# Kernel tuning notes

Hardware: AMD Instinct MI355X
Metric: run time of the kernel (lower is better)

The kernel has to match this reference:

```python
import jax, jax.numpy as jnp
import numpy as np

HID = 256
IN_DIM = 64
OUT_DIM = 4
B = 2048
T = 128


def setup_inputs() -> dict:
    key = jax.random.key(0)
    ks = jax.random.split(key, 12)
    s = lambda k, shp, fan: jax.random.normal(k, shp, jnp.float32) / np.sqrt(fan)
    return {
        "static_input": jax.random.normal(ks[0], (B, IN_DIM), jnp.float32),
        "times": jnp.arange(T, dtype=jnp.float32) * 0.05,  # increasing grid
        "W_in": s(ks[1], (IN_DIM, HID), IN_DIM), "b_in": jnp.zeros((HID,), jnp.float32),
        "W1": s(ks[2], (HID, HID), HID), "b1": jnp.zeros((HID,), jnp.float32),
        "W2": s(ks[3], (HID, HID), HID), "b2": jnp.zeros((HID,), jnp.float32),
        "W_pk": s(ks[4], (HID, OUT_DIM), HID), "b_pk": jnp.zeros((OUT_DIM,), jnp.float32),
        "W_pd": s(ks[5], (HID, 1), HID), "b_pd": jnp.zeros((1,), jnp.float32),
    }


def _odefunc(h, W1, b1, W2, b2):
    # Linear -> Tanh -> Linear (autonomous: ignores t, as in the torch ODEFunc)
    return jnp.tanh(h @ W1 + b1) @ W2 + b2


def reference(static_input, times, W_in, b_in, W1, b1, W2, b2, W_pk, b_pk, W_pd, b_pd):
    h0 = static_input @ W_in + b_in  # [B, H]
    f = lambda h: _odefunc(h, W1, b1, W2, b2)
    dts = times[1:] - times[:-1]  # [T-1]

    def rk4_step(h, dt):
        k1 = f(h)
        k2 = f(h + 0.5 * dt * k1)
        k3 = f(h + 0.5 * dt * k2)
        k4 = f(h + dt * k3)
        h_next = h + (dt / 6.0) * (k1 + 2.0 * k2 + 2.0 * k3 + k4)
        return h_next, h_next

    _, h_rest = jax.lax.scan(rk4_step, h0, dts)  # [T-1, B, H]
    h_ts = jnp.concatenate([h0[None], h_rest], axis=0)  # [T, B, H]
    h_ts = jnp.transpose(h_ts, (1, 0, 2))  # [B, T, H]
    pk_pred = h_ts @ W_pk + b_pk          # [B, T, OUT_DIM]
    pd_pred = h_ts[:, -1, :] @ W_pd + b_pd  # [B, 1]
    return (pk_pred, pd_pred)
```

## Files before the change

### kernel.cpp

```cpp
#include <hip/hip_runtime.h>
#include <hip/hip_bf16.h>
#include <stdint.h>

#define H       256
#define INDIM   64
#define TSTEPS  128
#define BATCH   2048
#define MROWS   8
#define OUTD    4

typedef __attribute__((ext_vector_type(8))) short bf16x8;
typedef __attribute__((ext_vector_type(4))) float f32x4;

__device__ __forceinline__ short b2s(float x) {
  __hip_bfloat16 h = __float2bfloat16(x);
  return __builtin_bit_cast(short, h);
}

__device__ __forceinline__ int swz(int m, int n) {
  return (m * H + n) ^ ((m & 7) << 3);
}

__device__ __forceinline__ float swap_hilo(float a, float b) {
#if __has_builtin(__builtin_amdgcn_permlane32_swap)
  typedef unsigned int u32x2 __attribute__((ext_vector_type(2)));
  u32x2 r = __builtin_amdgcn_permlane32_swap(
      __builtin_bit_cast(unsigned int, a),
      __builtin_bit_cast(unsigned int, b), false, false);
  return __builtin_bit_cast(float, r[0]);
#else
  float t = __shfl_xor(b, 32);
  return (threadIdx.x & 32) ? t : a;
#endif
}

__global__ __launch_bounds__(512, 1) void node_kernel(
    const float* __restrict__ g_static, const float* __restrict__ g_times,
    const float* __restrict__ g_Win, const float* __restrict__ g_bin,
    const float* __restrict__ g_W1, const float* __restrict__ g_b1,
    const float* __restrict__ g_W2, const float* __restrict__ g_b2,
    const float* __restrict__ g_Wpk, const float* __restrict__ g_bpk,
    const float* __restrict__ g_Wpd, const float* __restrict__ g_bpd,
    float* __restrict__ g_out)
{
  __shared__ __align__(16) short arg_lds[MROWS * H];
  __shared__ __align__(16) short h1_lds[MROWS * H];
  __shared__ __align__(16) short wpk_lds[8 * 64 * 8];
  __shared__ float h_lds[MROWS * H];
  __shared__ float s_lds[MROWS * INDIM];
  __shared__ float t_lds[TSTEPS];

  const int tid   = threadIdx.x;
  const int lane  = tid & 63;
  const int wid   = tid >> 6;
  const int g     = lane >> 4;
  const int c     = lane & 15;
  const int b0    = blockIdx.x * MROWS;
  const int ncol0 = wid * 32;
  const int am    = lane & 7;
  const int gg    = (lane >> 4) & 1;
  const int hh    = lane >> 5;
  const int colu  = ncol0 + 16 * hh + c;
  const int dm    = 4 * g;

  if (tid < TSTEPS) t_lds[tid] = g_times[tid];

  const float b1u2 = 2.0f * g_b1[colu];
  const float b2u  = g_b2[colu];
  const float bpkc = g_bpk[c & 3];
  const float bpdv = g_bpd[0];
  float wpd[4];
#pragma unroll
  for (int j = 0; j < 4; ++j) wpd[j] = g_Wpd[lane + 64 * j];

  int ra[8], wa[4], ha[4];
#pragma unroll
  for (int kt = 0; kt < 8; ++kt) ra[kt] = swz(am, kt * 32 + g * 8);
#pragma unroll
  for (int r = 0; r < 4; ++r) {
    wa[r] = swz(4 * gg + r, colu);
    ha[r] = (4 * gg + r) * H + colu;
  }

  bf16x8 w1f[8][2], w2f[8][2];
#pragma unroll
  for (int kt = 0; kt < 8; ++kt) {
#pragma unroll
    for (int nt = 0; nt < 2; ++nt) {
      const int n  = ncol0 + nt * 16 + c;
      const int kb = kt * 32 + g * 8;
      bf16x8 f1, f2;
#pragma unroll
      for (int u = 0; u < 8; ++u) {
        f1[u] = b2s(g_W1[(kb + u) * H + n]);
        f2[u] = b2s(g_W2[(kb + u) * H + n]);
      }
      w1f[kt][nt] = f1;
      w2f[kt][nt] = f2;
    }
  }

  if (wid == 0) {
#pragma unroll
    for (int kt = 0; kt < 8; ++kt) {
      bf16x8 f;
#pragma unroll
      for (int u = 0; u < 8; ++u) {
        const int k = kt * 32 + g * 8 + u;
        f[u] = (c < OUTD) ? b2s(g_Wpk[k * OUTD + c]) : (short)0;
      }
      *(bf16x8*)(wpk_lds + kt * 512 + lane * 8) = f;
    }
  }

  s_lds[tid] = g_static[(b0 + (tid >> 6)) * INDIM + (tid & 63)];
  __syncthreads();
  {
    const int m  = tid >> 6;
    const int n0 = (tid & 63) * 4;
    float a0 = g_bin[n0], a1 = g_bin[n0 + 1], a2 = g_bin[n0 + 2], a3 = g_bin[n0 + 3];
#pragma unroll 8
    for (int k = 0; k < INDIM; ++k) {
      const float sv = s_lds[m * INDIM + k];
      const f32x4 w = *(const f32x4*)(g_Win + k * H + n0);
      a0 += sv * w[0]; a1 += sv * w[1]; a2 += sv * w[2]; a3 += sv * w[3];
    }
    h_lds[m * H + n0] = a0;     h_lds[m * H + n0 + 1] = a1;
    h_lds[m * H + n0 + 2] = a2; h_lds[m * H + n0 + 3] = a3;
    arg_lds[swz(m, n0)]     = b2s(a0);
    arg_lds[swz(m, n0 + 1)] = b2s(a1);
    arg_lds[swz(m, n0 + 2)] = b2s(a2);
    arg_lds[swz(m, n0 + 3)] = b2s(a3);
  }
  __syncthreads();

  float hb[4];
#pragma unroll
  for (int r = 0; r < 4; ++r) hb[r] = h_lds[ha[r]];

  auto emit_pk = [&](int t) {
    if (wid == 0) {
      f32x4 acc = {0.f, 0.f, 0.f, 0.f};
#pragma unroll
      for (int kt = 0; kt < 8; ++kt) {
        const bf16x8 aA = *(const bf16x8*)(arg_lds + ra[kt]);
        const bf16x8 bW = *(const bf16x8*)(wpk_lds + kt * 512 + lane * 8);
        acc = __builtin_amdgcn_mfma_f32_16x16x32_bf16(aA, bW, acc, 0, 0, 0);
      }
      if (g < 2 && c < OUTD) {
#pragma unroll
        for (int r = 0; r < 4; ++r)
          g_out[((size_t)(b0 + dm + r) * TSTEPS + t) * OUTD + c] = acc[r] + bpkc;
      }
    }
  };

  emit_pk(0);

  for (int t = 1; t < TSTEPS; ++t) {
    const float dt = t_lds[t] - t_lds[t - 1];
    const float s6 = dt * (1.0f / 6.0f);
    float ks[4];

#pragma unroll
    for (int ev = 0; ev < 4; ++ev) {
      f32x4 A0 = {0.f,0.f,0.f,0.f}, A1 = {0.f,0.f,0.f,0.f};
      f32x4 B0 = {0.f,0.f,0.f,0.f}, B1 = {0.f,0.f,0.f,0.f};
#pragma unroll
      for (int kt = 0; kt < 4; ++kt) {
        const bf16x8 aA = *(const bf16x8*)(arg_lds + ra[kt]);
        const bf16x8 aB = *(const bf16x8*)(arg_lds + ra[kt + 4]);
        A0 = __builtin_amdgcn_mfma_f32_16x16x32_bf16(aA, w1f[kt][0], A0, 0, 0, 0);
        A1 = __builtin_amdgcn_mfma_f32_16x16x32_bf16(aA, w1f[kt][1], A1, 0, 0, 0);
        B0 = __builtin_amdgcn_mfma_f32_16x16x32_bf16(aB, w1f[kt + 4][0], B0, 0, 0, 0);
        B1 = __builtin_amdgcn_mfma_f32_16x16x32_bf16(aB, w1f[kt + 4][1], B1, 0, 0, 0);
      }
#pragma unroll
      for (int r = 0; r < 4; ++r) {
        const float v = swap_hilo(A0[r] + B0[r], A1[r] + B1[r]);
        const float e = __expf(__builtin_fmaf(2.0f, v, b1u2));
        const float th = 1.0f - __fdividef(2.0f, e + 1.0f);
        h1_lds[wa[r]] = b2s(th);
      }
      __syncthreads();

      A0 = f32x4{0.f,0.f,0.f,0.f}; A1 = f32x4{0.f,0.f,0.f,0.f};
      B0 = f32x4{0.f,0.f,0.f,0.f}; B1 = f32x4{0.f,0.f,0.f,0.f};
#pragma unroll
      for (int kt = 0; kt < 4; ++kt) {
        const bf16x8 aA = *(const bf16x8*)(h1_lds + ra[kt]);
        const bf16x8 aB = *(const bf16x8*)(h1_lds + ra[kt + 4]);
        A0 = __builtin_amdgcn_mfma_f32_16x16x32_bf16(aA, w2f[kt][0], A0, 0, 0, 0);
        A1 = __builtin_amdgcn_mfma_f32_16x16x32_bf16(aA, w2f[kt][1], A1, 0, 0, 0);
        B0 = __builtin_amdgcn_mfma_f32_16x16x32_bf16(aB, w2f[kt + 4][0], B0, 0, 0, 0);
        B1 = __builtin_amdgcn_mfma_f32_16x16x32_bf16(aB, w2f[kt + 4][1], B1, 0, 0, 0);
      }
#pragma unroll
      for (int r = 0; r < 4; ++r) {
        const float kv = swap_hilo(A0[r] + B0[r], A1[r] + B1[r]) + b2u;
        if (ev == 0)      ks[r] = kv;
        else if (ev == 3) ks[r] += kv;
        else              ks[r] += 2.0f * kv;
        if (ev < 3) {
          const float cc = (ev == 2) ? dt : 0.5f * dt;
          arg_lds[wa[r]] = b2s(__builtin_fmaf(cc, kv, hb[r]));
        } else {
          hb[r] = __builtin_fmaf(s6, ks[r], hb[r]);
          arg_lds[wa[r]] = b2s(hb[r]);
        }
      }
      __syncthreads();
    }
    emit_pk(t);
  }

#pragma unroll
  for (int r = 0; r < 4; ++r) h_lds[ha[r]] = hb[r];
  __syncthreads();
  {
    float p = 0.0f;
#pragma unroll
    for (int j = 0; j < 4; ++j) p += h_lds[wid * H + lane + 64 * j] * wpd[j];
#pragma unroll
    for (int m = 1; m < 64; m <<= 1) p += __shfl_xor(p, m);
    if (lane == 0) g_out[(size_t)BATCH * TSTEPS * OUTD + b0 + wid] = p + bpdv;
  }
}

extern "C" void kernel_launch(void* const* d_in, const int* in_sizes, int n_in,
                              void* d_out, int out_size, void* d_ws, size_t ws_size,
                              hipStream_t stream) {
  const float* g_static = (const float*)d_in[0];
  const float* g_times  = (const float*)d_in[1];
  const float* g_Win    = (const float*)d_in[2];
  const float* g_bin    = (const float*)d_in[3];
  const float* g_W1     = (const float*)d_in[4];
  const float* g_b1     = (const float*)d_in[5];
  const float* g_W2     = (const float*)d_in[6];
  const float* g_b2     = (const float*)d_in[7];
  const float* g_Wpk    = (const float*)d_in[8];
  const float* g_bpk    = (const float*)d_in[9];
  const float* g_Wpd    = (const float*)d_in[10];
  const float* g_bpd    = (const float*)d_in[11];

  node_kernel<<<dim3(BATCH / MROWS), dim3(512), 0, stream>>>(
      g_static, g_times, g_Win, g_bin, g_W1, g_b1, g_W2, g_b2,
      g_Wpk, g_bpk, g_Wpd, g_bpd, (float*)d_out);
}
```

Measured before the change: 660.7 us.

## Re-swizzle LDS layout for conflict-free loads and split MFMA accumulators into four chains

Replaces the XOR swizzle of the bf16 activation buffers with a new grouped index mapping, and permutes the Wpk LDS slots to match, aiming to remove LDS bank conflicts on the 16-byte fragment loads. The MFMA reduction now hoists all eight A-fragment loads up front and spreads the K dimension over four independent accumulator chains per output tile instead of two, to shorten dependent MFMA latency within each RK4 stage. This costs extra accumulator registers and a final vector add tree, and the new swizzle must stay consistent across all readers and writers.

```diff
diff --git a/kernel.cpp b/kernel.cpp
--- a/kernel.cpp
+++ b/kernel.cpp
@@ -17,8 +17,16 @@
   return __builtin_bit_cast(short, h);
 }
 
-__device__ __forceinline__ int swz(int m, int n) {
-  return (m * H + n) ^ ((m & 7) << 3);
+__device__ __forceinline__ int grp(int row, int kt, int g) {
+  return (((row ^ g) & 3) << 1) | (((g >> 1) ^ kt ^ (row >> 2)) & 1);
+}
+__device__ __forceinline__ int sidx(int row, int col) {
+  const int kt = col >> 5, g = (col >> 3) & 3, u = col & 7;
+  return row * 256 + ((kt >> 1) << 6) + grp(row, kt, g) * 8 + u;
+}
+__device__ __forceinline__ int wpk_slot(int lane) {
+  return (((lane & 3) << 1) | ((lane >> 4) & 1)) |
+         (((lane >> 2) & 3) << 3) | (((lane >> 5) & 1) << 5);
 }
 
 __device__ __forceinline__ float swap_hilo(float a, float b) {
@@ -33,6 +41,8 @@
   return (threadIdx.x & 32) ? t : a;
 #endif
 }
+
+#define MFMA(a, b, c) __builtin_amdgcn_mfma_f32_16x16x32_bf16((a), (b), (c), 0, 0, 0)
 
 __global__ __launch_bounds__(512, 1) void node_kernel(
     const float* __restrict__ g_static, const float* __restrict__ g_times,
@@ -75,10 +85,10 @@
 
   int ra[8], wa[4], ha[4];
 #pragma unroll
-  for (int kt = 0; kt < 8; ++kt) ra[kt] = swz(am, kt * 32 + g * 8);
+  for (int kt = 0; kt < 8; ++kt) ra[kt] = sidx(am, kt * 32 + g * 8);
 #pragma unroll
   for (int r = 0; r < 4; ++r) {
-    wa[r] = swz(4 * gg + r, colu);
+    wa[r] = sidx(4 * gg + r, colu);
     ha[r] = (4 * gg + r) * H + colu;
   }
 
@@ -101,6 +111,7 @@
   }
 
   if (wid == 0) {
+    const int slot = wpk_slot(lane);
 #pragma unroll
     for (int kt = 0; kt < 8; ++kt) {
       bf16x8 f;
@@ -109,7 +120,7 @@
         const int k = kt * 32 + g * 8 + u;
         f[u] = (c < OUTD) ? b2s(g_Wpk[k * OUTD + c]) : (short)0;
       }
-      *(bf16x8*)(wpk_lds + kt * 512 + lane * 8) = f;
+      *(bf16x8*)(wpk_lds + kt * 512 + slot * 8) = f;
     }
   }
 
@@ -127,10 +138,10 @@
     }
     h_lds[m * H + n0] = a0;     h_lds[m * H + n0 + 1] = a1;
     h_lds[m * H + n0 + 2] = a2; h_lds[m * H + n0 + 3] = a3;
-    arg_lds[swz(m, n0)]     = b2s(a0);
-    arg_lds[swz(m, n0 + 1)] = b2s(a1);
-    arg_lds[swz(m, n0 + 2)] = b2s(a2);
-    arg_lds[swz(m, n0 + 3)] = b2s(a3);
+    arg_lds[sidx(m, n0)]     = b2s(a0);
+    arg_lds[sidx(m, n0 + 1)] = b2s(a1);
+    arg_lds[sidx(m, n0 + 2)] = b2s(a2);
+    arg_lds[sidx(m, n0 + 3)] = b2s(a3);
   }
   __syncthreads();
 
@@ -138,14 +149,15 @@
 #pragma unroll
   for (int r = 0; r < 4; ++r) hb[r] = h_lds[ha[r]];
 
+  const int wslot = wpk_slot(lane);
   auto emit_pk = [&](int t) {
     if (wid == 0) {
       f32x4 acc = {0.f, 0.f, 0.f, 0.f};
 #pragma unroll
       for (int kt = 0; kt < 8; ++kt) {
         const bf16x8 aA = *(const bf16x8*)(arg_lds + ra[kt]);
-        const bf16x8 bW = *(const bf16x8*)(wpk_lds + kt * 512 + lane * 8);
-        acc = __builtin_amdgcn_mfma_f32_16x16x32_bf16(aA, bW, acc, 0, 0, 0);
+        const bf16x8 bW = *(const bf16x8*)(wpk_lds + kt * 512 + wslot * 8);
+        acc = MFMA(aA, bW, acc);
       }
       if (g < 2 && c < OUTD) {
 #pragma unroll
@@ -157,6 +169,7 @@
 
   emit_pk(0);
 
+  const f32x4 vz = {0.f, 0.f, 0.f, 0.f};
   for (int t = 1; t < TSTEPS; ++t) {
     const float dt = t_lds[t] - t_lds[t - 1];
     const float s6 = dt * (1.0f / 6.0f);
@@ -164,49 +177,71 @@
 
 #pragma unroll
     for (int ev = 0; ev < 4; ++ev) {
-      f32x4 A0 = {0.f,0.f,0.f,0.f}, A1 = {0.f,0.f,0.f,0.f};
-      f32x4 B0 = {0.f,0.f,0.f,0.f}, B1 = {0.f,0.f,0.f,0.f};
-#pragma unroll
-      for (int kt = 0; kt < 4; ++kt) {
-        const bf16x8 aA = *(const bf16x8*)(arg_lds + ra[kt]);
-        const bf16x8 aB = *(const bf16x8*)(arg_lds + ra[kt + 4]);
-        A0 = __builtin_amdgcn_mfma_f32_16x16x32_bf16(aA, w1f[kt][0], A0, 0, 0, 0);
-        A1 = __builtin_amdgcn_mfma_f32_16x16x32_bf16(aA, w1f[kt][1], A1, 0, 0, 0);
-        B0 = __builtin_amdgcn_mfma_f32_16x16x32_bf16(aB, w1f[kt + 4][0], B0, 0, 0, 0);
-        B1 = __builtin_amdgcn_mfma_f32_16x16x32_bf16(aB, w1f[kt + 4][1], B1, 0, 0, 0);
-      }
-#pragma unroll
-      for (int r = 0; r < 4; ++r) {
-        const float v = swap_hilo(A0[r] + B0[r], A1[r] + B1[r]);
-        const float e = __expf(__builtin_fmaf(2.0f, v, b1u2));
-        const float th = 1.0f - __fdividef(2.0f, e + 1.0f);
-        h1_lds[wa[r]] = b2s(th);
+      {
+        const bf16x8 f0 = *(const bf16x8*)(arg_lds + ra[0]);
+        const bf16x8 f1 = *(const bf16x8*)(arg_lds + ra[1]);
+        const bf16x8 f2 = *(const bf16x8*)(arg_lds + ra[2]);
+        const bf16x8 f3 = *(const bf16x8*)(arg_lds + ra[3]);
+        const bf16x8 f4 = *(const bf16x8*)(arg_lds + ra[4]);
+        const bf16x8 f5 = *(const bf16x8*)(arg_lds + ra[5]);
+        const bf16x8 f6 = *(const bf16x8*)(arg_lds + ra[6]);
+        const bf16x8 f7 = *(const bf16x8*)(arg_lds + ra[7]);
+        f32x4 c00 = vz, c01 = vz, c02 = vz, c03 = vz;
+        f32x4 c10 = vz, c11 = vz, c12 = vz, c13 = vz;
+        c00 = MFMA(f0, w1f[0][0], c00); c10 = MFMA(f0, w1f[0][1], c10);
+        c01 = MFMA(f2, w1f[2][0], c01); c11 = MFMA(f2, w1f[2][1], c11);
+        c02 = MFMA(f4, w1f[4][0], c02); c12 = MFMA(f4, w1f[4][1], c12);
+        c03 = MFMA(f6, w1f[6][0], c03); c13 = MFMA(f6, w1f[6][1], c13);
+        c00 = MFMA(f1, w1f[1][0], c00); c10 = MFMA(f1, w1f[1][1], c10);
+        c01 = MFMA(f3, w1f[3][0], c01); c11 = MFMA(f3, w1f[3][1], c11);
+        c02 = MFMA(f5, w1f[5][0], c02); c12 = MFMA(f5, w1f[5][1], c12);
+        c03 = MFMA(f7, w1f[7][0], c03); c13 = MFMA(f7, w1f[7][1], c13);
+        const f32x4 S0 = (c00 + c01) + (c02 + c03);
+        const f32x4 S1 = (c10 + c11) + (c12 + c13);
+#pragma unroll
+        for (int r = 0; r < 4; ++r) {
+          const float v = swap_hilo(S0[r], S1[r]);
+          const float e = __expf(__builtin_fmaf(2.0f, v, b1u2));
+          const float th = 1.0f - __fdividef(2.0f, e + 1.0f);
+          h1_lds[wa[r]] = b2s(th);
+        }
       }
       __syncthreads();
 
-      A0 = f32x4{0.f,0.f,0.f,0.f}; A1 = f32x4{0.f,0.f,0.f,0.f};
-      B0 = f32x4{0.f,0.f,0.f,0.f}; B1 = f32x4{0.f,0.f,0.f,0.f};
-#pragma unroll
-      for (int kt = 0; kt < 4; ++kt) {
-        const bf16x8 aA = *(const bf16x8*)(h1_lds + ra[kt]);
-        const bf16x8 aB = *(const bf16x8*)(h1_lds + ra[kt + 4]);
-        A0 = __builtin_amdgcn_mfma_f32_16x16x32_bf16(aA, w2f[kt][0], A0, 0, 0, 0);
-        A1 = __builtin_amdgcn_mfma_f32_16x16x32_bf16(aA, w2f[kt][1], A1, 0, 0, 0);
-        B0 = __builtin_amdgcn_mfma_f32_16x16x32_bf16(aB, w2f[kt + 4][0], B0, 0, 0, 0);
-        B1 = __builtin_amdgcn_mfma_f32_16x16x32_bf16(aB, w2f[kt + 4][1], B1, 0, 0, 0);
-      }
-#pragma unroll
-      for (int r = 0; r < 4; ++r) {
-        const float kv = swap_hilo(A0[r] + B0[r], A1[r] + B1[r]) + b2u;
-        if (ev == 0)      ks[r] = kv;
-        else if (ev == 3) ks[r] += kv;
-        else              ks[r] += 2.0f * kv;
-        if (ev < 3) {
-          const float cc = (ev == 2) ? dt : 0.5f * dt;
-          arg_lds[wa[r]] = b2s(__builtin_fmaf(cc, kv, hb[r]));
-        } else {
-          hb[r] = __builtin_fmaf(s6, ks[r], hb[r]);
-          arg_lds[wa[r]] = b2s(hb[r]);
+      {
+        const bf16x8 f0 = *(const bf16x8*)(h1_lds + ra[0]);
+        const bf16x8 f1 = *(const bf16x8*)(h1_lds + ra[1]);
+        const bf16x8 f2 = *(const bf16x8*)(h1_lds + ra[2]);
+        const bf16x8 f3 = *(const bf16x8*)(h1_lds + ra[3]);
+        const bf16x8 f4 = *(const bf16x8*)(h1_lds + ra[4]);
+        const bf16x8 f5 = *(const bf16x8*)(h1_lds + ra[5]);
+        const bf16x8 f6 = *(const bf16x8*)(h1_lds + ra[6]);
+        const bf16x8 f7 = *(const bf16x8*)(h1_lds + ra[7]);
+        f32x4 c00 = vz, c01 = vz, c02 = vz, c03 = vz;
+        f32x4 c10 = vz, c11 = vz, c12 = vz, c13 = vz;
+        c00 = MFMA(f0, w2f[0][0], c00); c10 = MFMA(f0, w2f[0][1], c10);
+        c01 = MFMA(f2, w2f[2][0], c01); c11 = MFMA(f2, w2f[2][1], c11);
+        c02 = MFMA(f4, w2f[4][0], c02); c12 = MFMA(f4, w2f[4][1], c12);
+        c03 = MFMA(f6, w2f[6][0], c03); c13 = MFMA(f6, w2f[6][1], c13);
+        c00 = MFMA(f1, w2f[1][0], c00); c10 = MFMA(f1, w2f[1][1], c10);
+        c01 = MFMA(f3, w2f[3][0], c01); c11 = MFMA(f3, w2f[3][1], c11);
+        c02 = MFMA(f5, w2f[5][0], c02); c12 = MFMA(f5, w2f[5][1], c12);
+        c03 = MFMA(f7, w2f[7][0], c03); c13 = MFMA(f7, w2f[7][1], c13);
+        const f32x4 S0 = (c00 + c01) + (c02 + c03);
+        const f32x4 S1 = (c10 + c11) + (c12 + c13);
+#pragma unroll
+        for (int r = 0; r < 4; ++r) {
+          const float kv = swap_hilo(S0[r], S1[r]) + b2u;
+          if (ev == 0)      ks[r] = kv;
+          else if (ev == 3) ks[r] += kv;
+          else              ks[r] += 2.0f * kv;
+          if (ev < 3) {
+            const float cc = (ev == 2) ? dt : 0.5f * dt;
+            arg_lds[wa[r]] = b2s(__builtin_fmaf(cc, kv, hb[r]));
+          } else {
+            hb[r] = __builtin_fmaf(s6, ks[r], hb[r]);
+            arg_lds[wa[r]] = b2s(hb[r]);
+          }
         }
       }
       __syncthreads();
```

Result: slower. 724.1 us (+9.6%).

## Halve block to 4 waves, each computing 64 columns with doubled register weights

Applied to the files above, without the earlier changes.

The block shrinks from 8 to 4 waves. Each wave now owns 64 output columns and holds 8x4 bf16 fragments of W1 and W2 in registers, with several pieces of state (hb, ks, write addresses) doubled to match. Biases are folded into the MFMA accumulator init instead of being added afterwards. The W_pk LDS slot mapping is permuted, and the input projection and final pd reduction are adjusted for 256 threads. The aim is to cut barrier and LDS-fragment-reload overhead per RK4 stage by giving each wave more MFMAs per A-fragment load. The cost is much higher VGPR pressure (256 weight vector registers) and less parallelism per block, which risks spills.

```diff
diff --git a/kernel.cpp b/kernel.cpp
--- a/kernel.cpp
+++ b/kernel.cpp
@@ -19,6 +19,10 @@
 
 __device__ __forceinline__ int swz(int m, int n) {
   return (m * H + n) ^ ((m & 7) << 3);
+}
+__device__ __forceinline__ int wpk_slot(int lane) {
+  return (((lane & 3) << 1) | ((lane >> 4) & 1)) |
+         (((lane >> 2) & 3) << 3) | (((lane >> 5) & 1) << 5);
 }
 
 __device__ __forceinline__ float swap_hilo(float a, float b) {
@@ -34,7 +38,9 @@
 #endif
 }
 
-__global__ __launch_bounds__(512, 1) void node_kernel(
+#define MFMA(a, b, c) __builtin_amdgcn_mfma_f32_16x16x32_bf16((a), (b), (c), 0, 0, 0)
+
+__global__ __launch_bounds__(256, 1) void node_kernel(
     const float* __restrict__ g_static, const float* __restrict__ g_times,
     const float* __restrict__ g_Win, const float* __restrict__ g_bin,
     const float* __restrict__ g_W1, const float* __restrict__ g_b1,
@@ -56,37 +62,43 @@
   const int g     = lane >> 4;
   const int c     = lane & 15;
   const int b0    = blockIdx.x * MROWS;
-  const int ncol0 = wid * 32;
+  const int ncol0 = wid * 64;
   const int am    = lane & 7;
   const int gg    = (lane >> 4) & 1;
   const int hh    = lane >> 5;
-  const int colu  = ncol0 + 16 * hh + c;
+  const int cu    = ncol0 + 16 * hh + c;
   const int dm    = 4 * g;
 
   if (tid < TSTEPS) t_lds[tid] = g_times[tid];
 
-  const float b1u2 = 2.0f * g_b1[colu];
-  const float b2u  = g_b2[colu];
+  float b1v[4], b2v[4];
+#pragma unroll
+  for (int nt = 0; nt < 4; ++nt) {
+    b1v[nt] = g_b1[ncol0 + nt * 16 + c];
+    b2v[nt] = g_b2[ncol0 + nt * 16 + c];
+  }
   const float bpkc = g_bpk[c & 3];
   const float bpdv = g_bpd[0];
   float wpd[4];
 #pragma unroll
   for (int j = 0; j < 4; ++j) wpd[j] = g_Wpd[lane + 64 * j];
 
-  int ra[8], wa[4], ha[4];
+  int ra[8], wa[2][4], ha[2][4];
 #pragma unroll
   for (int kt = 0; kt < 8; ++kt) ra[kt] = swz(am, kt * 32 + g * 8);
 #pragma unroll
-  for (int r = 0; r < 4; ++r) {
-    wa[r] = swz(4 * gg + r, colu);
-    ha[r] = (4 * gg + r) * H + colu;
-  }
-
-  bf16x8 w1f[8][2], w2f[8][2];
+  for (int p = 0; p < 2; ++p)
+#pragma unroll
+    for (int r = 0; r < 4; ++r) {
+      wa[p][r] = swz(4 * gg + r, cu + 32 * p);
+      ha[p][r] = (4 * gg + r) * H + cu + 32 * p;
+    }
+
+  bf16x8 w1f[8][4], w2f[8][4];
 #pragma unroll
   for (int kt = 0; kt < 8; ++kt) {
 #pragma unroll
-    for (int nt = 0; nt < 2; ++nt) {
+    for (int nt = 0; nt < 4; ++nt) {
       const int n  = ncol0 + nt * 16 + c;
       const int kb = kt * 32 + g * 8;
       bf16x8 f1, f2;
@@ -101,6 +113,7 @@
   }
 
   if (wid == 0) {
+    const int slot = wpk_slot(lane);
 #pragma unroll
     for (int kt = 0; kt < 8; ++kt) {
       bf16x8 f;
@@ -109,43 +122,53 @@
         const int k = kt * 32 + g * 8 + u;
         f[u] = (c < OUTD) ? b2s(g_Wpk[k * OUTD + c]) : (short)0;
       }
-      *(bf16x8*)(wpk_lds + kt * 512 + lane * 8) = f;
-    }
-  }
-
-  s_lds[tid] = g_static[(b0 + (tid >> 6)) * INDIM + (tid & 63)];
+      *(bf16x8*)(wpk_lds + kt * 512 + slot * 8) = f;
+    }
+  }
+
+  s_lds[tid]       = g_static[(b0 + (tid >> 6)) * INDIM + (tid & 63)];
+  s_lds[tid + 256] = g_static[(b0 + ((tid + 256) >> 6)) * INDIM + (tid & 63)];
   __syncthreads();
   {
-    const int m  = tid >> 6;
-    const int n0 = (tid & 63) * 4;
-    float a0 = g_bin[n0], a1 = g_bin[n0 + 1], a2 = g_bin[n0 + 2], a3 = g_bin[n0 + 3];
-#pragma unroll 8
+    const int m  = tid >> 5;
+    const int n0 = (tid & 31) * 8;
+    float a[8];
+#pragma unroll
+    for (int j = 0; j < 8; ++j) a[j] = g_bin[n0 + j];
+#pragma unroll 4
     for (int k = 0; k < INDIM; ++k) {
       const float sv = s_lds[m * INDIM + k];
-      const f32x4 w = *(const f32x4*)(g_Win + k * H + n0);
-      a0 += sv * w[0]; a1 += sv * w[1]; a2 += sv * w[2]; a3 += sv * w[3];
-    }
-    h_lds[m * H + n0] = a0;     h_lds[m * H + n0 + 1] = a1;
-    h_lds[m * H + n0 + 2] = a2; h_lds[m * H + n0 + 3] = a3;
-    arg_lds[swz(m, n0)]     = b2s(a0);
-    arg_lds[swz(m, n0 + 1)] = b2s(a1);
-    arg_lds[swz(m, n0 + 2)] = b2s(a2);
-    arg_lds[swz(m, n0 + 3)] = b2s(a3);
+      const f32x4 w0 = *(const f32x4*)(g_Win + k * H + n0);
+      const f32x4 w1 = *(const f32x4*)(g_Win + k * H + n0 + 4);
+#pragma unroll
+      for (int j = 0; j < 4; ++j) {
+        a[j]     += sv * w0[j];
+        a[j + 4] += sv * w1[j];
+      }
+    }
+#pragma unroll
+    for (int j = 0; j < 8; ++j) {
+      h_lds[m * H + n0 + j]     = a[j];
+      arg_lds[swz(m, n0 + j)]   = b2s(a[j]);
+    }
   }
   __syncthreads();
 
-  float hb[4];
-#pragma unroll
-  for (int r = 0; r < 4; ++r) hb[r] = h_lds[ha[r]];
-
+  float hb[2][4];
+#pragma unroll
+  for (int p = 0; p < 2; ++p)
+#pragma unroll
+    for (int r = 0; r < 4; ++r) hb[p][r] = h_lds[ha[p][r]];
+
+  const int wslot = wpk_slot(lane);
   auto emit_pk = [&](int t) {
     if (wid == 0) {
       f32x4 acc = {0.f, 0.f, 0.f, 0.f};
 #pragma unroll
       for (int kt = 0; kt < 8; ++kt) {
         const bf16x8 aA = *(const bf16x8*)(arg_lds + ra[kt]);
-        const bf16x8 bW = *(const bf16x8*)(wpk_lds + kt * 512 + lane * 8);
-        acc = __builtin_amdgcn_mfma_f32_16x16x32_bf16(aA, bW, acc, 0, 0, 0);
+        const bf16x8 bW = *(const bf16x8*)(wpk_lds + kt * 512 + wslot * 8);
+        acc = MFMA(aA, bW, acc);
       }
       if (g < 2 && c < OUTD) {
 #pragma unroll
@@ -157,57 +180,82 @@
 
   emit_pk(0);
 
+  const f32x4 vz = {0.f, 0.f, 0.f, 0.f};
   for (int t = 1; t < TSTEPS; ++t) {
     const float dt = t_lds[t] - t_lds[t - 1];
     const float s6 = dt * (1.0f / 6.0f);
-    float ks[4];
+    float ks[2][4];
 
 #pragma unroll
     for (int ev = 0; ev < 4; ++ev) {
-      f32x4 A0 = {0.f,0.f,0.f,0.f}, A1 = {0.f,0.f,0.f,0.f};
-      f32x4 B0 = {0.f,0.f,0.f,0.f}, B1 = {0.f,0.f,0.f,0.f};
-#pragma unroll
-      for (int kt = 0; kt < 4; ++kt) {
-        const bf16x8 aA = *(const bf16x8*)(arg_lds + ra[kt]);
-        const bf16x8 aB = *(const bf16x8*)(arg_lds + ra[kt + 4]);
-        A0 = __builtin_amdgcn_mfma_f32_16x16x32_bf16(aA, w1f[kt][0], A0, 0, 0, 0);
-        A1 = __builtin_amdgcn_mfma_f32_16x16x32_bf16(aA, w1f[kt][1], A1, 0, 0, 0);
-        B0 = __builtin_amdgcn_mfma_f32_16x16x32_bf16(aB, w1f[kt + 4][0], B0, 0, 0, 0);
-        B1 = __builtin_amdgcn_mfma_f32_16x16x32_bf16(aB, w1f[kt + 4][1], B1, 0, 0, 0);
-      }
-#pragma unroll
-      for (int r = 0; r < 4; ++r) {
-        const float v = swap_hilo(A0[r] + B0[r], A1[r] + B1[r]);
-        const float e = __expf(__builtin_fmaf(2.0f, v, b1u2));
-        const float th = 1.0f - __fdividef(2.0f, e + 1.0f);
-        h1_lds[wa[r]] = b2s(th);
+      {
+        f32x4 cA[4], cB[4];
+#pragma unroll
+        for (int nt = 0; nt < 4; ++nt) {
+          cA[nt] = f32x4{b1v[nt], b1v[nt], b1v[nt], b1v[nt]};
+          cB[nt] = vz;
+        }
+#pragma unroll
+        for (int kt = 0; kt < 4; ++kt) {
+          const bf16x8 fA = *(const bf16x8*)(arg_lds + ra[kt]);
+          const bf16x8 fB = *(const bf16x8*)(arg_lds + ra[kt + 4]);
+#pragma unroll
+          for (int nt = 0; nt < 4; ++nt) {
+            cA[nt] = MFMA(fA, w1f[kt][nt], cA[nt]);
+            cB[nt] = MFMA(fB, w1f[kt + 4][nt], cB[nt]);
+          }
+        }
+        f32x4 S[4];
+#pragma unroll
+        for (int nt = 0; nt < 4; ++nt) S[nt] = cA[nt] + cB[nt];
+#pragma unroll
+        for (int p = 0; p < 2; ++p)
+#pragma unroll
+          for (int r = 0; r < 4; ++r) {
+            const float v = swap_hilo(S[2 * p][r], S[2 * p + 1][r]);
+            const float e = __expf(2.0f * v);
+            const float th = 1.0f - __fdividef(2.0f, e + 1.0f);
+            h1_lds[wa[p][r]] = b2s(th);
+          }
       }
       __syncthreads();
 
-      A0 = f32x4{0.f,0.f,0.f,0.f}; A1 = f32x4{0.f,0.f,0.f,0.f};
-      B0 = f32x4{0.f,0.f,0.f,0.f}; B1 = f32x4{0.f,0.f,0.f,0.f};
-#pragma unroll
-      for (int kt = 0; kt < 4; ++kt) {
-        const bf16x8 aA = *(const bf16x8*)(h1_lds + ra[kt]);
-        const bf16x8 aB = *(const bf16x8*)(h1_lds + ra[kt + 4]);
-        A0 = __builtin_amdgcn_mfma_f32_16x16x32_bf16(aA, w2f[kt][0], A0, 0, 0, 0);
-        A1 = __builtin_amdgcn_mfma_f32_16x16x32_bf16(aA, w2f[kt][1], A1, 0, 0, 0);
-        B0 = __builtin_amdgcn_mfma_f32_16x16x32_bf16(aB, w2f[kt + 4][0], B0, 0, 0, 0);
-        B1 = __builtin_amdgcn_mfma_f32_16x16x32_bf16(aB, w2f[kt + 4][1], B1, 0, 0, 0);
-      }
-#pragma unroll
-      for (int r = 0; r < 4; ++r) {
-        const float kv = swap_hilo(A0[r] + B0[r], A1[r] + B1[r]) + b2u;
-        if (ev == 0)      ks[r] = kv;
-        else if (ev == 3) ks[r] += kv;
-        else              ks[r] += 2.0f * kv;
-        if (ev < 3) {
-          const float cc = (ev == 2) ? dt : 0.5f * dt;
-          arg_lds[wa[r]] = b2s(__builtin_fmaf(cc, kv, hb[r]));
-        } else {
-          hb[r] = __builtin_fmaf(s6, ks[r], hb[r]);
-          arg_lds[wa[r]] = b2s(hb[r]);
+      {
+        f32x4 cA[4], cB[4];
+#pragma unroll
+        for (int nt = 0; nt < 4; ++nt) {
+          cA[nt] = f32x4{b2v[nt], b2v[nt], b2v[nt], b2v[nt]};
+          cB[nt] = vz;
         }
+#pragma unroll
+        for (int kt = 0; kt < 4; ++kt) {
+          const bf16x8 fA = *(const bf16x8*)(h1_lds + ra[kt]);
+          const bf16x8 fB = *(const bf16x8*)(h1_lds + ra[kt + 4]);
+#pragma unroll
+          for (int nt = 0; nt < 4; ++nt) {
+            cA[nt] = MFMA(fA, w2f[kt][nt], cA[nt]);
+            cB[nt] = MFMA(fB, w2f[kt + 4][nt], cB[nt]);
+          }
+        }
+        f32x4 S[4];
+#pragma unroll
+        for (int nt = 0; nt < 4; ++nt) S[nt] = cA[nt] + cB[nt];
+#pragma unroll
+        for (int p = 0; p < 2; ++p)
+#pragma unroll
+          for (int r = 0; r < 4; ++r) {
+            const float kv = swap_hilo(S[2 * p][r], S[2 * p + 1][r]);
+            if (ev == 0)      ks[p][r] = kv;
+            else if (ev == 3) ks[p][r] += kv;
+            else              ks[p][r] += 2.0f * kv;
+            if (ev < 3) {
+              const float cc = (ev == 2) ? dt : 0.5f * dt;
+              arg_lds[wa[p][r]] = b2s(__builtin_fmaf(cc, kv, hb[p][r]));
+            } else {
+              hb[p][r] = __builtin_fmaf(s6, ks[p][r], hb[p][r]);
+              arg_lds[wa[p][r]] = b2s(hb[p][r]);
+            }
+          }
       }
       __syncthreads();
     }
@@ -215,15 +263,19 @@
   }
 
 #pragma unroll
-  for (int r = 0; r < 4; ++r) h_lds[ha[r]] = hb[r];
+  for (int p = 0; p < 2; ++p)
+#pragma unroll
+    for (int r = 0; r < 4; ++r) h_lds[ha[p][r]] = hb[p][r];
   __syncthreads();
-  {
+#pragma unroll
+  for (int rr = 0; rr < 2; ++rr) {
+    const int row = wid + 4 * rr;
     float p = 0.0f;
 #pragma unroll
-    for (int j = 0; j < 4; ++j) p += h_lds[wid * H + lane + 64 * j] * wpd[j];
+    for (int j = 0; j < 4; ++j) p += h_lds[row * H + lane + 64 * j] * wpd[j];
 #pragma unroll
     for (int m = 1; m < 64; m <<= 1) p += __shfl_xor(p, m);
-    if (lane == 0) g_out[(size_t)BATCH * TSTEPS * OUTD + b0 + wid] = p + bpdv;
+    if (lane == 0) g_out[(size_t)BATCH * TSTEPS * OUTD + b0 + row] = p + bpdv;
   }
 }
 
@@ -243,7 +295,7 @@
   const float* g_Wpd    = (const float*)d_in[10];
   const float* g_bpd    = (const float*)d_in[11];
 
-  node_kernel<<<dim3(BATCH / MROWS), dim3(512), 0, stream>>>(
+  node_kernel<<<dim3(BATCH / MROWS), dim3(256), 0, stream>>>(
       g_static, g_times, g_Win, g_bin, g_W1, g_b1, g_W2, g_b2,
       g_Wpk, g_bpk, g_Wpd, g_bpd, (float*)d_out);
 }
```

Result: slower. 924.1 us (+39.9%).

## Duplicate activation rows in LDS, new swizzle, and stagger K order per wave

Applied to the files above, without the earlier changes.

The bf16 activation buffers grow from 8 to 16 rows, with every row written twice so all 16 MFMA A-operand lanes read distinct addresses, and a new XOR swizzle folds the high row bit in. Odd-numbered waves walk the K tiles in rotated order and the register-resident weight fragments are permuted to match, which spreads LDS reads across banks between waves. The Wpk fragment slots are also permuted. This aims to cut LDS bank conflicts on the serial RK4 critical path, at the cost of doubling every LDS store.

```diff
diff --git a/kernel.cpp b/kernel.cpp
--- a/kernel.cpp
+++ b/kernel.cpp
@@ -17,8 +17,13 @@
   return __builtin_bit_cast(short, h);
 }
 
-__device__ __forceinline__ int swz(int m, int n) {
-  return (m * H + n) ^ ((m & 7) << 3);
+__device__ __forceinline__ int sidx16(int m, int n) {
+  const int smix = ((m & 7) ^ (m >> 3)) & 7;
+  return m * H + (n ^ (smix << 3));
+}
+__device__ __forceinline__ int wpk_slot(int lane) {
+  return (((lane & 3) << 1) | ((lane >> 4) & 1)) |
+         (((lane >> 2) & 3) << 3) | (((lane >> 5) & 1) << 5);
 }
 
 __device__ __forceinline__ float swap_hilo(float a, float b) {
@@ -34,6 +39,8 @@
 #endif
 }
 
+#define MFMA(a, b, c) __builtin_amdgcn_mfma_f32_16x16x32_bf16((a), (b), (c), 0, 0, 0)
+
 __global__ __launch_bounds__(512, 1) void node_kernel(
     const float* __restrict__ g_static, const float* __restrict__ g_times,
     const float* __restrict__ g_Win, const float* __restrict__ g_bin,
@@ -43,8 +50,8 @@
     const float* __restrict__ g_Wpd, const float* __restrict__ g_bpd,
     float* __restrict__ g_out)
 {
-  __shared__ __align__(16) short arg_lds[MROWS * H];
-  __shared__ __align__(16) short h1_lds[MROWS * H];
+  __shared__ __align__(16) short arg_lds[16 * H];
+  __shared__ __align__(16) short h1_lds[16 * H];
   __shared__ __align__(16) short wpk_lds[8 * 64 * 8];
   __shared__ float h_lds[MROWS * H];
   __shared__ float s_lds[MROWS * INDIM];
@@ -57,7 +64,7 @@
   const int c     = lane & 15;
   const int b0    = blockIdx.x * MROWS;
   const int ncol0 = wid * 32;
-  const int am    = lane & 7;
+  const int am    = lane & 15;
   const int gg    = (lane >> 4) & 1;
   const int hh    = lane >> 5;
   const int colu  = ncol0 + 16 * hh + c;
@@ -73,18 +80,25 @@
 #pragma unroll
   for (int j = 0; j < 4; ++j) wpd[j] = g_Wpd[lane + 64 * j];
 
-  int ra[8], wa[4], ha[4];
-#pragma unroll
-  for (int kt = 0; kt < 8; ++kt) ra[kt] = swz(am, kt * 32 + g * 8);
+  const int ko = (wid & 1) ? 4 : 0;
+  int ra[8];
+#pragma unroll
+  for (int i = 0; i < 4; ++i) {
+    ra[i]     = sidx16(am, (ko + i) * 32 + g * 8);
+    ra[i + 4] = sidx16(am, ((ko ^ 4) + i) * 32 + g * 8);
+  }
+  int wlo[4], whi[4], ha[4];
 #pragma unroll
   for (int r = 0; r < 4; ++r) {
-    wa[r] = swz(4 * gg + r, colu);
-    ha[r] = (4 * gg + r) * H + colu;
+    wlo[r] = sidx16(4 * gg + r, colu);
+    whi[r] = sidx16(4 * gg + r + 8, colu);
+    ha[r]  = (4 * gg + r) * H + colu;
   }
 
   bf16x8 w1f[8][2], w2f[8][2];
 #pragma unroll
-  for (int kt = 0; kt < 8; ++kt) {
+  for (int i = 0; i < 8; ++i) {
+    const int kt = (i < 4) ? (ko + i) : ((ko ^ 4) + i - 4);
 #pragma unroll
     for (int nt = 0; nt < 2; ++nt) {
       const int n  = ncol0 + nt * 16 + c;
@@ -95,12 +109,13 @@
         f1[u] = b2s(g_W1[(kb + u) * H + n]);
         f2[u] = b2s(g_W2[(kb + u) * H + n]);
       }
-      w1f[kt][nt] = f1;
-      w2f[kt][nt] = f2;
+      w1f[i][nt] = f1;
+      w2f[i][nt] = f2;
     }
   }
 
   if (wid == 0) {
+    const int slot = wpk_slot(lane);
 #pragma unroll
     for (int kt = 0; kt < 8; ++kt) {
       bf16x8 f;
@@ -109,7 +124,7 @@
         const int k = kt * 32 + g * 8 + u;
         f[u] = (c < OUTD) ? b2s(g_Wpk[k * OUTD + c]) : (short)0;
       }
-      *(bf16x8*)(wpk_lds + kt * 512 + lane * 8) = f;
+      *(bf16x8*)(wpk_lds + kt * 512 + slot * 8) = f;
     }
   }
 
@@ -127,10 +142,12 @@
     }
     h_lds[m * H + n0] = a0;     h_lds[m * H + n0 + 1] = a1;
     h_lds[m * H + n0 + 2] = a2; h_lds[m * H + n0 + 3] = a3;
-    arg_lds[swz(m, n0)]     = b2s(a0);
-    arg_lds[swz(m, n0 + 1)] = b2s(a1);
-    arg_lds[swz(m, n0 + 2)] = b2s(a2);
-    arg_lds[swz(m, n0 + 3)] = b2s(a3);
+    const float av[4] = {a0, a1, a2, a3};
+#pragma unroll
+    for (int j = 0; j < 4; ++j) {
+      arg_lds[sidx16(m, n0 + j)]     = b2s(av[j]);
+      arg_lds[sidx16(m + 8, n0 + j)] = b2s(av[j]);
+    }
   }
   __syncthreads();
 
@@ -138,14 +155,15 @@
 #pragma unroll
   for (int r = 0; r < 4; ++r) hb[r] = h_lds[ha[r]];
 
+  const int wslot = wpk_slot(lane);
   auto emit_pk = [&](int t) {
     if (wid == 0) {
       f32x4 acc = {0.f, 0.f, 0.f, 0.f};
 #pragma unroll
       for (int kt = 0; kt < 8; ++kt) {
         const bf16x8 aA = *(const bf16x8*)(arg_lds + ra[kt]);
-        const bf16x8 bW = *(const bf16x8*)(wpk_lds + kt * 512 + lane * 8);
-        acc = __builtin_amdgcn_mfma_f32_16x16x32_bf16(aA, bW, acc, 0, 0, 0);
+        const bf16x8 bW = *(const bf16x8*)(wpk_lds + kt * 512 + wslot * 8);
+        acc = MFMA(aA, bW, acc);
       }
       if (g < 2 && c < OUTD) {
 #pragma unroll
@@ -157,6 +175,7 @@
 
   emit_pk(0);
 
+  const f32x4 vz = {0.f, 0.f, 0.f, 0.f};
   for (int t = 1; t < TSTEPS; ++t) {
     const float dt = t_lds[t] - t_lds[t - 1];
     const float s6 = dt * (1.0f / 6.0f);
@@ -164,49 +183,60 @@
 
 #pragma unroll
     for (int ev = 0; ev < 4; ++ev) {
-      f32x4 A0 = {0.f,0.f,0.f,0.f}, A1 = {0.f,0.f,0.f,0.f};
-      f32x4 B0 = {0.f,0.f,0.f,0.f}, B1 = {0.f,0.f,0.f,0.f};
-#pragma unroll
-      for (int kt = 0; kt < 4; ++kt) {
-        const bf16x8 aA = *(const bf16x8*)(arg_lds + ra[kt]);
-        const bf16x8 aB = *(const bf16x8*)(arg_lds + ra[kt + 4]);
-        A0 = __builtin_amdgcn_mfma_f32_16x16x32_bf16(aA, w1f[kt][0], A0, 0, 0, 0);
-        A1 = __builtin_amdgcn_mfma_f32_16x16x32_bf16(aA, w1f[kt][1], A1, 0, 0, 0);
-        B0 = __builtin_amdgcn_mfma_f32_16x16x32_bf16(aB, w1f[kt + 4][0], B0, 0, 0, 0);
-        B1 = __builtin_amdgcn_mfma_f32_16x16x32_bf16(aB, w1f[kt + 4][1], B1, 0, 0, 0);
-      }
-#pragma unroll
-      for (int r = 0; r < 4; ++r) {
-        const float v = swap_hilo(A0[r] + B0[r], A1[r] + B1[r]);
-        const float e = __expf(__builtin_fmaf(2.0f, v, b1u2));
-        const float th = 1.0f - __fdividef(2.0f, e + 1.0f);
-        h1_lds[wa[r]] = b2s(th);
+      {
+        f32x4 A0 = vz, A1 = vz, B0 = vz, B1 = vz;
+#pragma unroll
+        for (int i = 0; i < 4; ++i) {
+          const bf16x8 fA = *(const bf16x8*)(arg_lds + ra[i]);
+          const bf16x8 fB = *(const bf16x8*)(arg_lds + ra[i + 4]);
+          A0 = MFMA(fA, w1f[i][0], A0);
+          A1 = MFMA(fA, w1f[i][1], A1);
+          B0 = MFMA(fB, w1f[i + 4][0], B0);
+          B1 = MFMA(fB, w1f[i + 4][1], B1);
+        }
+        const f32x4 S0 = A0 + B0;
+        const f32x4 S1 = A1 + B1;
+#pragma unroll
+        for (int r = 0; r < 4; ++r) {
+          const float v  = swap_hilo(S0[r], S1[r]);
+          const float e  = __expf(__builtin_fmaf(2.0f, v, b1u2));
+          const float th = 1.0f - __fdividef(2.0f, e + 1.0f);
+          const short sv = b2s(th);
+          h1_lds[wlo[r]] = sv;
+          h1_lds[whi[r]] = sv;
+        }
       }
       __syncthreads();
 
-      A0 = f32x4{0.f,0.f,0.f,0.f}; A1 = f32x4{0.f,0.f,0.f,0.f};
-      B0 = f32x4{0.f,0.f,0.f,0.f}; B1 = f32x4{0.f,0.f,0.f,0.f};
-#pragma unroll
-      for (int kt = 0; kt < 4; ++kt) {
-        const bf16x8 aA = *(const bf16x8*)(h1_lds + ra[kt]);
-        const bf16x8 aB = *(const bf16x8*)(h1_lds + ra[kt + 4]);
-        A0 = __builtin_amdgcn_mfma_f32_16x16x32_bf16(aA, w2f[kt][0], A0, 0, 0, 0);
-        A1 = __builtin_amdgcn_mfma_f32_16x16x32_bf16(aA, w2f[kt][1], A1, 0, 0, 0);
-        B0 = __builtin_amdgcn_mfma_f32_16x16x32_bf16(aB, w2f[kt + 4][0], B0, 0, 0, 0);
-        B1 = __builtin_amdgcn_mfma_f32_16x16x32_bf16(aB, w2f[kt + 4][1], B1, 0, 0, 0);
-      }
-#pragma unroll
-      for (int r = 0; r < 4; ++r) {
-        const float kv = swap_hilo(A0[r] + B0[r], A1[r] + B1[r]) + b2u;
-        if (ev == 0)      ks[r] = kv;
-        else if (ev == 3) ks[r] += kv;
-        else              ks[r] += 2.0f * kv;
-        if (ev < 3) {
-          const float cc = (ev == 2) ? dt : 0.5f * dt;
-          arg_lds[wa[r]] = b2s(__builtin_fmaf(cc, kv, hb[r]));
-        } else {
-          hb[r] = __builtin_fmaf(s6, ks[r], hb[r]);
-          arg_lds[wa[r]] = b2s(hb[r]);
+      {
+        f32x4 A0 = vz, A1 = vz, B0 = vz, B1 = vz;
+#pragma unroll
+        for (int i = 0; i < 4; ++i) {
+          const bf16x8 fA = *(const bf16x8*)(h1_lds + ra[i]);
+          const bf16x8 fB = *(const bf16x8*)(h1_lds + ra[i + 4]);
+          A0 = MFMA(fA, w2f[i][0], A0);
+          A1 = MFMA(fA, w2f[i][1], A1);
+          B0 = MFMA(fB, w2f[i + 4][0], B0);
+          B1 = MFMA(fB, w2f[i + 4][1], B1);
+        }
+        const f32x4 S0 = A0 + B0;
+        const f32x4 S1 = A1 + B1;
+#pragma unroll
+        for (int r = 0; r < 4; ++r) {
+          const float kv = swap_hilo(S0[r], S1[r]) + b2u;
+          if (ev == 0)      ks[r] = kv;
+          else if (ev == 3) ks[r] += kv;
+          else              ks[r] += 2.0f * kv;
+          short sv;
+          if (ev < 3) {
+            const float cc = (ev == 2) ? dt : 0.5f * dt;
+            sv = b2s(__builtin_fmaf(cc, kv, hb[r]));
+          } else {
+            hb[r] = __builtin_fmaf(s6, ks[r], hb[r]);
+            sv = b2s(hb[r]);
+          }
+          arg_lds[wlo[r]] = sv;
+          arg_lds[whi[r]] = sv;
         }
       }
       __syncthreads();
```

Result: slower. 686.9 us (+4.0%).
